# Kernel tuning notes

Hardware: AMD Instinct MI355X
Metric: run time of the kernel (lower is better)

The kernel has to match this reference:

```python
import jax, jax.numpy as jnp
import numpy as np

NUM_HEAD = 16
D_MODEL = 1024


def setup_inputs() -> dict:
    key = jax.random.key(0)
    k1, k2, k3 = jax.random.split(key, 3)
    B, S = 4, 2048
    x = jax.random.normal(k1, (B, S, D_MODEL), dtype=jnp.float32)
    W_qkv = jax.random.normal(k2, (D_MODEL, 3 * D_MODEL), dtype=jnp.float32) * (D_MODEL ** -0.5)
    b_qkv = jnp.zeros((3 * D_MODEL,), dtype=jnp.float32)
    W_o = jax.random.normal(k3, (D_MODEL, D_MODEL), dtype=jnp.float32) * (D_MODEL ** -0.5)
    b_o = jnp.zeros((D_MODEL,), dtype=jnp.float32)
    return {"x": x, "W_qkv": W_qkv, "b_qkv": b_qkv, "W_o": W_o, "b_o": b_o}


def reference(x, W_qkv, b_qkv, W_o, b_o):
    B, S, dm = x.shape
    H = NUM_HEAD
    hd = dm // H
    qkv = x @ W_qkv + b_qkv                       # [B,S,3*dm]
    qkv = qkv.reshape(B, S, H, 3 * hd).transpose(0, 2, 1, 3)  # [B,H,S,3*hd]
    q, k, v = jnp.split(qkv, 3, axis=-1)          # each [B,H,S,hd]
    scale = jnp.sqrt(jnp.asarray(hd, dtype=q.dtype))
    att = jnp.einsum('bhqd,bhkd->bhqk', q, k) / scale  # [B,H,S,S]
    causal = jnp.tril(jnp.ones((S, S), dtype=bool))    # band_part(ones,-1,0)
    att = jnp.where(causal, att, -jnp.inf)             # additive 0 / -inf mask
    att = jax.nn.softmax(att, axis=-1)
    vals = jnp.einsum('bhqk,bhkd->bhqd', att, v)       # [B,H,S,hd]
    # Faithful to original: reshape WITHOUT transposing heads back (axis scramble)
    vals = vals.reshape(B, S, H * hd)
    return vals @ W_o + b_o
```

## Files before the change

kernel.cpp:

```cpp
#include <hip/hip_runtime.h>
#include <hip/hip_bf16.h>
#include <stdint.h>


typedef __attribute__((ext_vector_type(8))) __bf16 bf16x8;
typedef __attribute__((ext_vector_type(4))) float f32x4;
typedef __attribute__((ext_vector_type(16))) float f32x16;

#define AS_G __attribute__((address_space(1)))
#define AS_L __attribute__((address_space(3)))

__device__ __forceinline__ void gload_lds16(const void* g, void* s) {
  __builtin_amdgcn_global_load_lds((const AS_G void*)g, (AS_L void*)s, 16, 0, 0);
}

__device__ __forceinline__ unsigned cvt_pk_bf16(float lo, float hi) {
  unsigned r;
  asm("v_cvt_pk_bf16_f32 %0, %1, %2" : "=v"(r) : "v"(lo), "v"(hi));
  return r;
}

__global__ void cvt_bf16_kernel(const float* __restrict__ in,
                                __bf16* __restrict__ out, int n8) {
  int i = blockIdx.x * blockDim.x + threadIdx.x;
  if (i >= n8) return;
  float4 a = ((const float4*)in)[i * 2];
  float4 b = ((const float4*)in)[i * 2 + 1];
  union { __bf16 h[8]; int4 v; } u;
  u.h[0] = (__bf16)a.x; u.h[1] = (__bf16)a.y; u.h[2] = (__bf16)a.z; u.h[3] = (__bf16)a.w;
  u.h[4] = (__bf16)b.x; u.h[5] = (__bf16)b.y; u.h[6] = (__bf16)b.z; u.h[7] = (__bf16)b.w;
  ((int4*)out)[i] = u.v;
}

__global__ void cvt_T_kernel(const float* __restrict__ in,
                             __bf16* __restrict__ out, int K, int N) {
  __shared__ float tile[32][33];
  int bx = blockIdx.x;
  int by = blockIdx.y;
  int tx = threadIdx.x & 31, ty = threadIdx.x >> 5;
#pragma unroll
  for (int i = 0; i < 32; i += 8)
    tile[ty + i][tx] = in[(size_t)(by * 32 + ty + i) * N + bx * 32 + tx];
  __syncthreads();
#pragma unroll
  for (int i = 0; i < 32; i += 8)
    out[(size_t)(bx * 32 + ty + i) * K + by * 32 + tx] = (__bf16)tile[tx][ty + i];
}

template <int MODE>
__global__ __launch_bounds__(512, 1) void gemm256(
    const __bf16* __restrict__ A, const __bf16* __restrict__ Bt,
    const float* __restrict__ bias,
    __bf16* __restrict__ Qb, __bf16* __restrict__ Kb, __bf16* __restrict__ Vtb,
    float* __restrict__ Out) {
  __shared__ char lds[98304];
  const int tid = threadIdx.x;
  const int wv = tid >> 6, lane = tid & 63;
  const int lhi = lane >> 4, llo = lane & 15;
  const int wm = wv >> 1, wn = wv & 1;

  const int wg = blockIdx.x;
  const int xcd = wg & 7, local = wg >> 3;
  const int m0 = (xcd * 4 + (local & 3)) * 256;
  const int n0 = (local >> 2) * 128;

  int SA[2], SB;
#pragma unroll
  for (int j = 0; j < 2; ++j) {
    const int idx = j * 512 + tid;
    const int v = idx >> 3, wl = idx & 7;
    const int wg_ = wl ^ (v & 7);
    SA[j] = ((v << 1) | (wg_ >> 2)) * 1024 + (wg_ & 3) * 8;
  }
  {
    const int v = tid >> 3, wl = tid & 7;
    const int wg_ = wl ^ (v & 7);
    SB = ((v << 1) | (wg_ >> 2)) * 1024 + (wg_ & 3) * 8;
  }
  const __bf16* Asrc = A + (size_t)m0 * 1024;
  const __bf16* Bsrc = Bt + (size_t)n0 * 1024;
  const int wvb = wv * 1024;

#define STAGE_AB(c, t, ks)                                                  \
  gload_lds16(Asrc + SA[0] + (t) * 64 + (ks) * 32,                          \
              &lds[(c) * 32768 + (ks) * 16384 + wvb]);                      \
  gload_lds16(Asrc + SA[1] + (t) * 64 + (ks) * 32,                          \
              &lds[(c) * 32768 + (ks) * 16384 + 8192 + wvb]);               \
  gload_lds16(Bsrc + SB + (t) * 64 + (ks) * 32,                             \
              &lds[65536 + (c) * 16384 + (ks) * 8192 + wvb]);

  f32x4 acc[4][4];
#pragma unroll
  for (int mi = 0; mi < 4; ++mi)
#pragma unroll
    for (int nj = 0; nj < 4; ++nj) acc[mi][nj] = (f32x4){0.f, 0.f, 0.f, 0.f};

  auto aoff = [&](int c, int ks, int f) {
    const int r = wm * 64 + f * 16 + llo;
    const int v = r >> 1;
    const int w = ((r & 1) << 2) | lhi;
    return c * 32768 + ks * 16384 + v * 128 + ((w ^ (v & 7)) << 4);
  };
  auto boff = [&](int c, int ks, int f2) {
    const int r = wn * 64 + f2 * 16 + llo;
    const int v = r >> 1;
    const int w = ((r & 1) << 2) | lhi;
    return 65536 + c * 16384 + ks * 8192 + v * 128 + ((w ^ (v & 7)) << 4);
  };

  auto PH = [&](int c, int ks, int sc, int st, int sks) {
    bf16x8 fa[4], fb[4];
#pragma unroll
    for (int f = 0; f < 4; ++f) fa[f] = *(const bf16x8*)&lds[aoff(c, ks, f)];
#pragma unroll
    for (int f2 = 0; f2 < 4; ++f2) fb[f2] = *(const bf16x8*)&lds[boff(c, ks, f2)];
    STAGE_AB(sc, st, sks);
    __builtin_amdgcn_sched_barrier(0);
    __builtin_amdgcn_s_barrier();
    asm volatile("s_waitcnt lgkmcnt(0)" ::: "memory");
    __builtin_amdgcn_sched_barrier(0);
    __builtin_amdgcn_s_setprio(1);
#pragma unroll
    for (int mi = 0; mi < 4; ++mi)
#pragma unroll
      for (int nj = 0; nj < 4; ++nj)
        acc[mi][nj] = __builtin_amdgcn_mfma_f32_16x16x32_bf16(fa[mi], fb[nj],
                                                              acc[mi][nj], 0, 0, 0);
    __builtin_amdgcn_s_setprio(0);
    __builtin_amdgcn_sched_barrier(0);
    asm volatile("s_waitcnt vmcnt(6)" ::: "memory");
    __builtin_amdgcn_s_barrier();
  };

  STAGE_AB(0, 0, 0);
  STAGE_AB(0, 0, 1);
  STAGE_AB(1, 1, 0);
  __builtin_amdgcn_sched_barrier(0);
  asm volatile("s_waitcnt vmcnt(6)" ::: "memory");
  __builtin_amdgcn_s_barrier();

  for (int j = 0; j < 8; ++j) {
    const int t1 = 2 * j + 1, t2 = (2 * j + 2) & 15, t3 = (2 * j + 3) & 15;
    PH(0, 0, 1, t1, 1);
    PH(0, 1, 0, t2, 0);
    PH(1, 0, 0, t2, 1);
    PH(1, 1, 1, t3, 0);
  }
#undef STAGE_AB

#pragma unroll
  for (int nj = 0; nj < 4; ++nj) {
    const int col = n0 + wn * 64 + nj * 16 + llo;
    const float bv = bias[col];
    if (MODE == 0) {
      const int h = col / 192, rem = col % 192;
#pragma unroll
      for (int mi = 0; mi < 4; ++mi) {
        const int row0 = m0 + wm * 64 + mi * 16 + lhi * 4;
        const int b = row0 >> 11;
        const int s0 = row0 & 2047;
        const int bh = b * 16 + h;
        f32x4 v = acc[mi][nj];
        if (rem < 64) {
#pragma unroll
          for (int r = 0; r < 4; ++r)
            Qb[((size_t)bh * 2048 + s0 + r) * 64 + rem] =
                (__bf16)((v[r] + bv) * 0.18033688011112042f);
        } else if (rem < 128) {
#pragma unroll
          for (int r = 0; r < 4; ++r)
            Kb[((size_t)bh * 2048 + s0 + r) * 64 + (rem - 64)] = (__bf16)(v[r] + bv);
        } else {
          union { __bf16 h4[4]; int2 v2; } uq;
#pragma unroll
          for (int r = 0; r < 4; ++r) uq.h4[r] = (__bf16)(v[r] + bv);
          *(int2*)&Vtb[((size_t)bh * 64 + (rem - 128)) * 2048 + s0] = uq.v2;
        }
      }
    } else {
#pragma unroll
      for (int mi = 0; mi < 4; ++mi) {
        const int row0 = m0 + wm * 64 + mi * 16 + lhi * 4;
        f32x4 v = acc[mi][nj];
#pragma unroll
        for (int r = 0; r < 4; ++r)
          Out[(size_t)(row0 + r) * 1024 + col] = v[r] + bv;
      }
    }
  }
}


__device__ __forceinline__ void attn_tile(
    const __bf16* __restrict__ ksb, const __bf16* __restrict__ vsb,
    const bf16x8* qf, const f32x16& zz, int kv0, int q0w, int lq, int hi,
    f32x16& o0, f32x16& o1, float& l) {
  const int r0 = lq, r1 = 32 + lq;
  const int fx = (lq & 7) ^ ((lq >> 3) << 1);
  f32x16 s0, s1;
  __builtin_amdgcn_s_setprio(1);
  {
    const int bb = (hi ^ fx) * 8;
    bf16x8 k0 = *(const bf16x8*)&ksb[r0 * 64 + bb];
    bf16x8 k1 = *(const bf16x8*)&ksb[r1 * 64 + bb];
    s0 = __builtin_amdgcn_mfma_f32_32x32x16_bf16(k0, qf[0], zz, 0, 0, 0);
    s1 = __builtin_amdgcn_mfma_f32_32x32x16_bf16(k1, qf[0], zz, 0, 0, 0);
  }
#pragma unroll
  for (int ds = 1; ds < 4; ++ds) {
    const int bb = ((ds * 2 + hi) ^ fx) * 8;
    bf16x8 k0 = *(const bf16x8*)&ksb[r0 * 64 + bb];
    bf16x8 k1 = *(const bf16x8*)&ksb[r1 * 64 + bb];
    s0 = __builtin_amdgcn_mfma_f32_32x32x16_bf16(k0, qf[ds], s0, 0, 0, 0);
    s1 = __builtin_amdgcn_mfma_f32_32x32x16_bf16(k1, qf[ds], s1, 0, 0, 0);
  }
  __builtin_amdgcn_s_setprio(0);

  const int qg = q0w + lq;
  if (kv0 + 63 > q0w) {
#pragma unroll
    for (int reg = 0; reg < 16; ++reg) {
      const int kvl = (reg & 3) + 8 * (reg >> 2) + 4 * hi;
      if (kv0 + kvl > qg) s0[reg] = -1e30f;
      if (kv0 + 32 + kvl > qg) s1[reg] = -1e30f;
    }
  }
#pragma unroll
  for (int i = 0; i < 16; ++i) s0[i] = __builtin_amdgcn_exp2f(s0[i]);
#pragma unroll
  for (int i = 0; i < 16; ++i) s1[i] = __builtin_amdgcn_exp2f(s1[i]);
  float y[8];
#pragma unroll
  for (int i = 0; i < 8; ++i) y[i] = (s0[i] + s0[i + 8]) + (s1[i] + s1[i + 8]);
#pragma unroll
  for (int st = 4; st; st >>= 1)
#pragma unroll
    for (int i = 0; i < st; ++i) y[i] += y[i + st];
  l += y[0] + __shfl_xor(y[0], 32);

#pragma unroll
  for (int ks = 0; ks < 4; ++ks) {
    unsigned pa, pb, pc, pd;
    if (ks < 2) {
      pa = cvt_pk_bf16(s0[ks * 8 + 0], s0[ks * 8 + 1]);
      pb = cvt_pk_bf16(s0[ks * 8 + 2], s0[ks * 8 + 3]);
      pc = cvt_pk_bf16(s0[ks * 8 + 4], s0[ks * 8 + 5]);
      pd = cvt_pk_bf16(s0[ks * 8 + 6], s0[ks * 8 + 7]);
    } else {
      pa = cvt_pk_bf16(s1[(ks - 2) * 8 + 0], s1[(ks - 2) * 8 + 1]);
      pb = cvt_pk_bf16(s1[(ks - 2) * 8 + 2], s1[(ks - 2) * 8 + 3]);
      pc = cvt_pk_bf16(s1[(ks - 2) * 8 + 4], s1[(ks - 2) * 8 + 5]);
      pd = cvt_pk_bf16(s1[(ks - 2) * 8 + 6], s1[(ks - 2) * 8 + 7]);
    }
    asm volatile("v_permlane32_swap_b32 %0, %1" : "+v"(pa), "+v"(pc));
    asm volatile("v_permlane32_swap_b32 %0, %1" : "+v"(pb), "+v"(pd));
    union { unsigned u[4]; bf16x8 v; } pf;
    pf.u[0] = pa; pf.u[1] = pb; pf.u[2] = pc; pf.u[3] = pd;
    const int vb = ((ks * 2 + hi) ^ fx) * 8;
    bf16x8 v0 = *(const bf16x8*)&vsb[r0 * 64 + vb];
    bf16x8 v1 = *(const bf16x8*)&vsb[r1 * 64 + vb];
    o0 = __builtin_amdgcn_mfma_f32_32x32x16_bf16(v0, pf.v, o0, 0, 0, 0);
    o1 = __builtin_amdgcn_mfma_f32_32x32x16_bf16(v1, pf.v, o1, 0, 0, 0);
  }
}

__device__ __forceinline__ void attn_epilogue(
    __bf16* __restrict__ vals, int bh, int q0w, int lq, int hi,
    const f32x16& o0, const f32x16& o1, float l) {
  const float inv = 1.f / l;
  unsigned* outp = (unsigned*)(vals + ((size_t)bh * 2048 + q0w + lq) * 64);
#pragma unroll
  for (int n = 0; n < 2; ++n) {
#pragma unroll
    for (int g = 0; g < 2; ++g) {
      const float e0 = (n ? o1[g * 8 + 0] : o0[g * 8 + 0]) * inv;
      const float e1 = (n ? o1[g * 8 + 1] : o0[g * 8 + 1]) * inv;
      const float e2 = (n ? o1[g * 8 + 2] : o0[g * 8 + 2]) * inv;
      const float e3 = (n ? o1[g * 8 + 3] : o0[g * 8 + 3]) * inv;
      const float e4 = (n ? o1[g * 8 + 4] : o0[g * 8 + 4]) * inv;
      const float e5 = (n ? o1[g * 8 + 5] : o0[g * 8 + 5]) * inv;
      const float e6 = (n ? o1[g * 8 + 6] : o0[g * 8 + 6]) * inv;
      const float e7 = (n ? o1[g * 8 + 7] : o0[g * 8 + 7]) * inv;
      unsigned a = cvt_pk_bf16(e0, e1);
      unsigned a2 = cvt_pk_bf16(e2, e3);
      unsigned b = cvt_pk_bf16(e4, e5);
      unsigned b2 = cvt_pk_bf16(e6, e7);
      asm volatile("v_permlane32_swap_b32 %0, %1" : "+v"(a), "+v"(b));
      asm volatile("v_permlane32_swap_b32 %0, %1" : "+v"(a2), "+v"(b2));
      int4 st = {(int)a, (int)a2, (int)b, (int)b2};
      *(int4*)&outp[(n * 32 + g * 16 + hi * 8) >> 1] = st;
    }
  }
}

__global__ __launch_bounds__(256) void attn_kernel(
    const __bf16* __restrict__ Q, const __bf16* __restrict__ K,
    const __bf16* __restrict__ Vt, __bf16* __restrict__ vals) {
  __shared__ __bf16 Ks[2][4096];
  __shared__ __bf16 Vs[2][4096];
  const int tid = threadIdx.x;
  const int wave = tid >> 6, lane = tid & 63;
  const int lq = lane & 31, hi = lane >> 5;

  const int wg = blockIdx.x + (blockIdx.y << 3);
  const int wgid = (wg & 7) * 128 + (wg >> 3);
  const int local = wgid & 127;
  const int bh = (wgid >> 7) * 8 + (local & 7);
  const int qc = 15 - (local >> 3);
  const int q0w = qc * 128 + wave * 32;
  const int nt = 2 * qc + 2;

  bf16x8 qf[4];
  {
    const __bf16* qp = Q + ((size_t)bh * 2048 + q0w + lq) * 64 + hi * 8;
#pragma unroll
    for (int ds = 0; ds < 4; ++ds) qf[ds] = *(const bf16x8*)(qp + ds * 16);
  }

  f32x16 o0, o1, zz;
#pragma unroll
  for (int i = 0; i < 16; ++i) { o0[i] = 0.f; o1[i] = 0.f; zz[i] = 0.f; }
  float l = 0.f;

  const int sr = tid >> 3, sb_ = tid & 7;
  const int sc = (sb_ ^ ((sr & 7) ^ ((sr >> 3) << 1))) * 8;
  const __bf16* Kg0 = K + ((size_t)bh * 2048 + sr) * 64 + sc;
  const __bf16* Kg1 = Kg0 + 32 * 64;
  const __bf16* Vg0 = Vt + ((size_t)bh * 64 + sr) * 2048 + sc;
  const __bf16* Vg1 = Vg0 + 32 * 2048;
  __bf16* KsW = &Ks[0][0] + wave * 512;
  __bf16* VsW = &Vs[0][0] + wave * 512;

#define STAGE(buf, t)                                                   \
  gload_lds16(Kg0 + (size_t)(t) * 4096, KsW + (buf) * 4096);            \
  gload_lds16(Kg1 + (size_t)(t) * 4096, KsW + (buf) * 4096 + 2048);     \
  gload_lds16(Vg0 + (t) * 64, VsW + (buf) * 4096);                      \
  gload_lds16(Vg1 + (t) * 64, VsW + (buf) * 4096 + 2048);

  STAGE(0, 0);
  __syncthreads();

  for (int t = 0; t < nt; ++t) {
    const int cur = t & 1;
    if (t + 1 < nt) { STAGE(cur ^ 1, t + 1); }
    attn_tile(&Ks[cur][0], &Vs[cur][0], qf, zz, t * 64, q0w, lq, hi, o0, o1, l);
    __syncthreads();
  }
#undef STAGE

  attn_epilogue(vals, bh, q0w, lq, hi, o0, o1, l);
}

extern "C" void kernel_launch(void* const* d_in, const int* in_sizes, int n_in,
                              void* d_out, int out_size, void* d_ws, size_t ws_size,
                              hipStream_t stream) {
  const float* x = (const float*)d_in[0];
  const float* Wqkv = (const float*)d_in[1];
  const float* bqkv = (const float*)d_in[2];
  const float* Wo = (const float*)d_in[3];
  const float* bo = (const float*)d_in[4];
  float* out = (float*)d_out;
  char* ws = (char*)d_ws;

  __bf16* xb  = (__bf16*)(ws);
  __bf16* Wqt = (__bf16*)(ws + 16777216);
  __bf16* Wot = (__bf16*)(ws + 23068672);
  __bf16* Qb  = (__bf16*)(ws + 25165824);
  __bf16* Kb  = (__bf16*)(ws + 41943040);
  __bf16* Vtb = (__bf16*)(ws + 58720256);
  __bf16* vals = xb;

  cvt_bf16_kernel<<<4096, 256, 0, stream>>>(x, xb, 1048576);
  cvt_T_kernel<<<dim3(96, 32), 256, 0, stream>>>(Wqkv, Wqt, 1024, 3072);
  cvt_T_kernel<<<dim3(32, 32), 256, 0, stream>>>(Wo, Wot, 1024, 1024);
  gemm256<0><<<768, 512, 0, stream>>>(xb, Wqt, bqkv, Qb, Kb, Vtb, nullptr);
  attn_kernel<<<dim3(8, 128), 256, 0, stream>>>(Qb, Kb, Vtb, vals);
  gemm256<1><<<256, 512, 0, stream>>>(vals, Wot, bo, nullptr, nullptr, nullptr, out);
}
```

Measured before the change: 159.9 us.

## Switch GEMM to triple-buffered full-K-tile pipeline with fewer barriers

Restructures the bf16 GEMM main loop from a double-buffered half-K-tile pipeline (four phases per pair of K tiles) into a three-stage ring of full 64-wide K tiles. Each phase reads both k-halves of fragments and issues 32 MFMAs per barrier pair, while prefetching two tiles ahead. LDS grows from 96 KB to 144 KB and register pressure for fragments doubles. The aim is to halve barrier count per K tile and deepen latency hiding of global-to-LDS loads.

```diff
diff --git a/kernel.cpp b/kernel.cpp
--- a/kernel.cpp
+++ b/kernel.cpp
@@ -53,7 +53,7 @@
     const float* __restrict__ bias,
     __bf16* __restrict__ Qb, __bf16* __restrict__ Kb, __bf16* __restrict__ Vtb,
     float* __restrict__ Out) {
-  __shared__ char lds[98304];
+  __shared__ char lds[147456];
   const int tid = threadIdx.x;
   const int wv = tid >> 6, lane = tid & 63;
   const int lhi = lane >> 4, llo = lane & 15;
@@ -81,13 +81,13 @@
   const __bf16* Bsrc = Bt + (size_t)n0 * 1024;
   const int wvb = wv * 1024;
 
-#define STAGE_AB(c, t, ks)                                                  \
-  gload_lds16(Asrc + SA[0] + (t) * 64 + (ks) * 32,                          \
-              &lds[(c) * 32768 + (ks) * 16384 + wvb]);                      \
-  gload_lds16(Asrc + SA[1] + (t) * 64 + (ks) * 32,                          \
-              &lds[(c) * 32768 + (ks) * 16384 + 8192 + wvb]);               \
-  gload_lds16(Bsrc + SB + (t) * 64 + (ks) * 32,                             \
-              &lds[65536 + (c) * 16384 + (ks) * 8192 + wvb]);
+#define STAGE_AB(c, t)                                                      \
+  gload_lds16(Asrc + SA[0] + (t) * 64,      &lds[(c) * 32768 + wvb]);       \
+  gload_lds16(Asrc + SA[1] + (t) * 64,      &lds[(c) * 32768 + 8192 + wvb]);\
+  gload_lds16(Asrc + SA[0] + (t) * 64 + 32, &lds[(c) * 32768 + 16384 + wvb]);\
+  gload_lds16(Asrc + SA[1] + (t) * 64 + 32, &lds[(c) * 32768 + 24576 + wvb]);\
+  gload_lds16(Bsrc + SB + (t) * 64,         &lds[98304 + (c) * 16384 + wvb]);\
+  gload_lds16(Bsrc + SB + (t) * 64 + 32,    &lds[98304 + (c) * 16384 + 8192 + wvb]);
 
   f32x4 acc[4][4];
 #pragma unroll
@@ -105,46 +105,53 @@
     const int r = wn * 64 + f2 * 16 + llo;
     const int v = r >> 1;
     const int w = ((r & 1) << 2) | lhi;
-    return 65536 + c * 16384 + ks * 8192 + v * 128 + ((w ^ (v & 7)) << 4);
+    return 98304 + c * 16384 + ks * 8192 + v * 128 + ((w ^ (v & 7)) << 4);
   };
 
-  auto PH = [&](int c, int ks, int sc, int st, int sks) {
-    bf16x8 fa[4], fb[4];
-#pragma unroll
-    for (int f = 0; f < 4; ++f) fa[f] = *(const bf16x8*)&lds[aoff(c, ks, f)];
-#pragma unroll
-    for (int f2 = 0; f2 < 4; ++f2) fb[f2] = *(const bf16x8*)&lds[boff(c, ks, f2)];
-    STAGE_AB(sc, st, sks);
+  auto PH = [&](int c, int sc, int st) {
+    bf16x8 fa[2][4], fb[2][4];
+#pragma unroll
+    for (int ks = 0; ks < 2; ++ks)
+#pragma unroll
+      for (int f = 0; f < 4; ++f) fa[ks][f] = *(const bf16x8*)&lds[aoff(c, ks, f)];
+#pragma unroll
+    for (int ks = 0; ks < 2; ++ks)
+#pragma unroll
+      for (int f2 = 0; f2 < 4; ++f2) fb[ks][f2] = *(const bf16x8*)&lds[boff(c, ks, f2)];
+    STAGE_AB(sc, st);
     __builtin_amdgcn_sched_barrier(0);
     __builtin_amdgcn_s_barrier();
     asm volatile("s_waitcnt lgkmcnt(0)" ::: "memory");
+    asm volatile("s_waitcnt vmcnt(6)" ::: "memory");
     __builtin_amdgcn_sched_barrier(0);
     __builtin_amdgcn_s_setprio(1);
 #pragma unroll
-    for (int mi = 0; mi < 4; ++mi)
-#pragma unroll
-      for (int nj = 0; nj < 4; ++nj)
-        acc[mi][nj] = __builtin_amdgcn_mfma_f32_16x16x32_bf16(fa[mi], fb[nj],
-                                                              acc[mi][nj], 0, 0, 0);
+    for (int ks = 0; ks < 2; ++ks)
+#pragma unroll
+      for (int mi = 0; mi < 4; ++mi)
+#pragma unroll
+        for (int nj = 0; nj < 4; ++nj)
+          acc[mi][nj] = __builtin_amdgcn_mfma_f32_16x16x32_bf16(
+              fa[ks][mi], fb[ks][nj], acc[mi][nj], 0, 0, 0);
     __builtin_amdgcn_s_setprio(0);
     __builtin_amdgcn_sched_barrier(0);
-    asm volatile("s_waitcnt vmcnt(6)" ::: "memory");
     __builtin_amdgcn_s_barrier();
   };
 
-  STAGE_AB(0, 0, 0);
-  STAGE_AB(0, 0, 1);
-  STAGE_AB(1, 1, 0);
+  STAGE_AB(0, 0);
+  STAGE_AB(1, 1);
   __builtin_amdgcn_sched_barrier(0);
   asm volatile("s_waitcnt vmcnt(6)" ::: "memory");
   __builtin_amdgcn_s_barrier();
 
-  for (int j = 0; j < 8; ++j) {
-    const int t1 = 2 * j + 1, t2 = (2 * j + 2) & 15, t3 = (2 * j + 3) & 15;
-    PH(0, 0, 1, t1, 1);
-    PH(0, 1, 0, t2, 0);
-    PH(1, 0, 0, t2, 1);
-    PH(1, 1, 1, t3, 0);
+  {
+    int c = 0;
+    for (int p = 0; p < 16; ++p) {
+      const int sc = (c + 2) % 3;
+      PH(c, sc, (p + 2) & 15);
+      c = (c + 1) % 3;
+      if (c == 3) c = 0;
+    }
   }
 #undef STAGE_AB
 
```

Result: slower. 164.8 us (+3.1%).

## Restructure GEMM LDS pipeline into a 3-slot ring buffer with smaller LDS

Applied to the files above, without the earlier changes.

Replaces the 4-slot (2 chunks x 2 k-halves) LDS staging scheme with a 3-slot rotating ring of 32-wide K chunks. This cuts LDS from 96KB to 72KB, and launch bounds change from 1 to 4 blocks per CU as an occupancy hint. The prefetch distance drops to two chunks ahead, so vmcnt waits change to 3 outstanding loads. Each phase now rotates slot indices at runtime rather than using a compile-time unrolled pattern. The shallower prefetch can expose more memory latency, and the runtime slot indices add address arithmetic.

```diff
diff --git a/kernel.cpp b/kernel.cpp
--- a/kernel.cpp
+++ b/kernel.cpp
@@ -48,12 +48,12 @@
 }
 
 template <int MODE>
-__global__ __launch_bounds__(512, 1) void gemm256(
+__global__ __launch_bounds__(512, 4) void gemm256(
     const __bf16* __restrict__ A, const __bf16* __restrict__ Bt,
     const float* __restrict__ bias,
     __bf16* __restrict__ Qb, __bf16* __restrict__ Kb, __bf16* __restrict__ Vtb,
     float* __restrict__ Out) {
-  __shared__ char lds[98304];
+  __shared__ char lds[73728];
   const int tid = threadIdx.x;
   const int wv = tid >> 6, lane = tid & 63;
   const int lhi = lane >> 4, llo = lane & 15;
@@ -81,13 +81,10 @@
   const __bf16* Bsrc = Bt + (size_t)n0 * 1024;
   const int wvb = wv * 1024;
 
-#define STAGE_AB(c, t, ks)                                                  \
-  gload_lds16(Asrc + SA[0] + (t) * 64 + (ks) * 32,                          \
-              &lds[(c) * 32768 + (ks) * 16384 + wvb]);                      \
-  gload_lds16(Asrc + SA[1] + (t) * 64 + (ks) * 32,                          \
-              &lds[(c) * 32768 + (ks) * 16384 + 8192 + wvb]);               \
-  gload_lds16(Bsrc + SB + (t) * 64 + (ks) * 32,                             \
-              &lds[65536 + (c) * 16384 + (ks) * 8192 + wvb]);
+#define STAGE_R(b, kc)                                                      \
+  gload_lds16(Asrc + SA[0] + (kc) * 32, &lds[(b) * 16384 + wvb]);           \
+  gload_lds16(Asrc + SA[1] + (kc) * 32, &lds[(b) * 16384 + 8192 + wvb]);    \
+  gload_lds16(Bsrc + SB + (kc) * 32,    &lds[49152 + (b) * 8192 + wvb]);
 
   f32x4 acc[4][4];
 #pragma unroll
@@ -95,26 +92,26 @@
 #pragma unroll
     for (int nj = 0; nj < 4; ++nj) acc[mi][nj] = (f32x4){0.f, 0.f, 0.f, 0.f};
 
-  auto aoff = [&](int c, int ks, int f) {
+  auto aoff = [&](int b, int f) {
     const int r = wm * 64 + f * 16 + llo;
     const int v = r >> 1;
     const int w = ((r & 1) << 2) | lhi;
-    return c * 32768 + ks * 16384 + v * 128 + ((w ^ (v & 7)) << 4);
+    return b * 16384 + v * 128 + ((w ^ (v & 7)) << 4);
   };
-  auto boff = [&](int c, int ks, int f2) {
+  auto boff = [&](int b, int f2) {
     const int r = wn * 64 + f2 * 16 + llo;
     const int v = r >> 1;
     const int w = ((r & 1) << 2) | lhi;
-    return 65536 + c * 16384 + ks * 8192 + v * 128 + ((w ^ (v & 7)) << 4);
+    return 49152 + b * 8192 + v * 128 + ((w ^ (v & 7)) << 4);
   };
 
-  auto PH = [&](int c, int ks, int sc, int st, int sks) {
+  auto PH = [&](int c, int sb, int kc) {
     bf16x8 fa[4], fb[4];
 #pragma unroll
-    for (int f = 0; f < 4; ++f) fa[f] = *(const bf16x8*)&lds[aoff(c, ks, f)];
-#pragma unroll
-    for (int f2 = 0; f2 < 4; ++f2) fb[f2] = *(const bf16x8*)&lds[boff(c, ks, f2)];
-    STAGE_AB(sc, st, sks);
+    for (int f = 0; f < 4; ++f) fa[f] = *(const bf16x8*)&lds[aoff(c, f)];
+#pragma unroll
+    for (int f2 = 0; f2 < 4; ++f2) fb[f2] = *(const bf16x8*)&lds[boff(c, f2)];
+    STAGE_R(sb, kc);
     __builtin_amdgcn_sched_barrier(0);
     __builtin_amdgcn_s_barrier();
     asm volatile("s_waitcnt lgkmcnt(0)" ::: "memory");
@@ -128,25 +125,26 @@
                                                               acc[mi][nj], 0, 0, 0);
     __builtin_amdgcn_s_setprio(0);
     __builtin_amdgcn_sched_barrier(0);
-    asm volatile("s_waitcnt vmcnt(6)" ::: "memory");
+    asm volatile("s_waitcnt vmcnt(3)" ::: "memory");
     __builtin_amdgcn_s_barrier();
   };
 
-  STAGE_AB(0, 0, 0);
-  STAGE_AB(0, 0, 1);
-  STAGE_AB(1, 1, 0);
+  STAGE_R(0, 0);
+  STAGE_R(1, 1);
   __builtin_amdgcn_sched_barrier(0);
-  asm volatile("s_waitcnt vmcnt(6)" ::: "memory");
+  asm volatile("s_waitcnt vmcnt(3)" ::: "memory");
   __builtin_amdgcn_s_barrier();
 
-  for (int j = 0; j < 8; ++j) {
-    const int t1 = 2 * j + 1, t2 = (2 * j + 2) & 15, t3 = (2 * j + 3) & 15;
-    PH(0, 0, 1, t1, 1);
-    PH(0, 1, 0, t2, 0);
-    PH(1, 0, 0, t2, 1);
-    PH(1, 1, 1, t3, 0);
-  }
-#undef STAGE_AB
+  {
+    int c = 0, sb = 2;
+    for (int p = 0; p < 32; ++p) {
+      const int kc = (p + 2) & 31;
+      PH(c, sb, kc);
+      if (++c == 3) c = 0;
+      if (++sb == 3) sb = 0;
+    }
+  }
+#undef STAGE_R
 
 #pragma unroll
   for (int nj = 0; nj < 4; ++nj) {
```

After: 158.4 us. About the same (-0.9%).
